# Kernel optimization log

Hardware: AMD Instinct MI355X
Metric: run time of the kernel (lower is better)

Reference implementation:

```python
import jax, jax.numpy as jnp
import numpy as np
from jax import lax

EPSILON = 1e-12


def _sobel_kernels(n1=1, n2=2, n3=2):
    Sx = np.asarray([[[-n1, 0, n1], [-n2, 0, n2], [-n1, 0, n1]],
                     [[-n2, 0, n2], [-n3 * n2, 0, n3 * n2], [-n2, 0, n2]],
                     [[-n1, 0, n1], [-n2, 0, n2], [-n1, 0, n1]]])
    Sy = np.asarray([[[-n1, -n2, -n1], [0, 0, 0], [n1, n2, n1]],
                     [[-n2, -n3 * n2, -n2], [0, 0, 0], [n2, n3 * n2, n2]],
                     [[-n1, -n2, -n1], [0, 0, 0], [n1, n2, n1]]])
    Sz = np.asarray([[[-n1, -n2, -n1], [-n2, -n3 * n2, -n2], [-n1, -n2, -n1]],
                     [[0, 0, 0], [0, 0, 0], [0, 0, 0]],
                     [[n1, n2, n1], [n2, n3 * n2, n2], [n1, n2, n1]]])
    Sd11 = np.asarray([[[0, n1, n2], [-n1, 0, n1], [-n2, -n1, 0]],
                       [[0, n2, n2 * n3], [-n2, 0, n2], [-n2 * n3, -n2, 0]],
                       [[0, n1, n2], [-n1, 0, n1], [-n2, -n1, 0]]])
    Sd12 = np.asarray([[[-n2, -n1, 0], [-n1, 0, n1], [0, n1, n2]],
                       [[-n2 * n3, -n2, 0], [-n2, 0, n2], [0, n2, n2 * n3]],
                       [[-n2, -n1, 0], [-n1, 0, n1], [0, n1, n2]]])
    Sd21 = Sd11.T
    Sd22 = Sd12.T
    Sd31 = np.asarray([-S.T for S in Sd11.T])
    Sd32 = np.asarray([S.T for S in Sd12.T])
    ks = np.stack([Sx, Sy, Sz, Sd11, Sd12, Sd21, Sd22, Sd31, Sd32]).astype(np.float32)
    return jnp.asarray(ks[:, None])  # [9, 1, 3, 3, 3] (OIDHW)


_KERNELS = _sobel_kernels(1, 2, 2)


def _edge_magnitude(img):
    # img: [B, C, H, W, D]. Per-channel convs are summed over C in the original;
    # by linearity of conv, sum channels first, then run all 9 stencils at once.
    C = img.shape[1]
    x = jnp.sum(img, axis=1, keepdims=True)  # [B, 1, H, W, D]
    g = lax.conv_general_dilated(
        x, _KERNELS, window_strides=(1, 1, 1), padding='SAME',
        dimension_numbers=('NCDHW', 'OIDHW', 'NCDHW'))  # [B, 9, H, W, D]
    mag = jnp.sqrt(jnp.sum(g * g, axis=1, keepdims=True) + EPSILON)
    return mag / C  # (1/C) * sqrt(sum_sq + eps), matches operator precedence


def setup_inputs() -> dict:
    key = jax.random.key(0)
    k1, k2 = jax.random.split(key)
    shape = (2, 2, 128, 128, 128)
    y = jax.random.normal(k1, shape, dtype=jnp.float32)
    yp = jax.random.normal(k2, shape, dtype=jnp.float32)
    return {"y": y, "yp": yp}


def reference(y, yp):
    y_edge = _edge_magnitude(y)
    yp_edge = _edge_magnitude(yp)
    return jnp.mean((y_edge - yp_edge) ** 2)  # nn.MSELoss default 'mean'
```

## Files before the change

kernel.cpp:

```cpp
#include <hip/hip_runtime.h>


namespace {

typedef float v2f __attribute__((ext_vector_type(2)));

constexpr int ZDIM = 128, YDIM = 128, XDIM = 128;
constexpr int TX = 64, TY = 4, ZC = 16;
constexpr int OTW = 62;
constexpr int NXT = 3;
constexpr int YX = YDIM * XDIM;
constexpr size_t CS = (size_t)ZDIM * YX;
constexpr float INV_N = 1.0f / 4194304.0f;

__device__ __forceinline__ float bperm(int addr, float v) {
  return __int_as_float(__builtin_amdgcn_ds_bpermute(addr, __float_as_int(v)));
}

__device__ __forceinline__ v2f vfma(v2f a, v2f b, v2f c) {
  return __builtin_elementwise_fma(a, b, c);
}

__device__ __forceinline__ v2f vsplat(float x) { v2f r = {x, x}; return r; }

__device__ __forceinline__ v2f emag_ss(const v2f* __restrict__ Ca,
                                       const v2f* __restrict__ Cb,
                                       const v2f* __restrict__ Cc) {
  const v2f two = vsplat(2.0f);
  const v2f g1  = vfma(two, Cb[0], Ca[0] + Cc[0]);
  const v2f g2  = vfma(two, Cb[1], Ca[1] + Cc[1]);
  const v2f g3  = Cc[2] - Ca[2];
  const v2f Azx = vfma(two, Cb[3], Ca[3] + Cc[3]);
  const v2f Azy = vfma(two, Cb[4], Ca[4] + Cc[4]);
  const v2f Axz = Cc[5] - Ca[5];
  const v2f Axy = g2 - Cb[1];
  const v2f Ayx = g1 - Cb[0];
  const v2f Ayz = Cc[6] - Ca[6];
  const v2f g4 = Azx - Azy, g5 = Azx + Azy;
  const v2f g6 = Axz - Axy, g7 = Axz + Axy;
  const v2f g8 = Ayx - Ayz, g9 = Ayx + Ayz;
  v2f s = vfma(g1, g1, vsplat(1e-12f));
  s = vfma(g2, g2, s); s = vfma(g3, g3, s);
  s = vfma(g4, g4, s); s = vfma(g5, g5, s);
  s = vfma(g6, g6, s); s = vfma(g7, g7, s);
  s = vfma(g8, g8, s); s = vfma(g9, g9, s);
  return s;
}

__global__ __launch_bounds__(256)
void gme_loss_kernel(const float* __restrict__ y,
                     const float* __restrict__ yp,
                     float* __restrict__ out) {
  const int lane = threadIdx.x;
  const int ty   = threadIdx.y;
  const int tid  = ty * TX + lane;

  const int bx = blockIdx.x;
  const int t  = bx % NXT;
  const int yt = bx / NXT;
  const int yy = yt * TY + ty;
  const int z0 = blockIdx.y * ZC;
  const int b  = blockIdx.z;

  const float* Y0 = y  + (size_t)b * 2 * CS;
  const float* Y1 = Y0 + CS;
  const float* P0 = yp + (size_t)b * 2 * CS;
  const float* P1 = P0 + CS;

  const int  X0  = OTW * t - 1;
  const int  xg  = X0 + lane;
  const int  xgc = xg < 0 ? 0 : (xg > XDIM - 1 ? XDIM - 1 : xg);
  const bool xok = (unsigned)xg < (unsigned)XDIM;
  const bool eok = xok && (lane >= 1) && (lane <= OTW);
  const float xmask = xok ? 1.0f : 0.0f;
  const float emask = eok ? 1.0f : 0.0f;

  const int yM = yy > 0 ? yy - 1 : 0;
  const int yP = yy < YDIM - 1 ? yy + 1 : YDIM - 1;
  const int voxM = yM * XDIM + xgc;
  const int voxC = yy * XDIM + xgc;
  const int voxP = yP * XDIM + xgc;
  const float mm = (yy > 0) ? 1.0f : 0.0f;
  const float mp = (yy < YDIM - 1) ? 1.0f : 0.0f;

  const int addrL = (lane > 0 ? lane - 1 : 0) << 2;
  const int addrR = (lane < TX - 1 ? lane + 1 : TX - 1) << 2;

  v2f pf[3][6];
  v2f K[3][7] = {};
  float acc = 0.0f;

  auto loadRaw = [&](int buf, int zc) {
    const int zca = zc < 0 ? 0 : (zc > ZDIM - 1 ? ZDIM - 1 : zc);
    const int o   = zca * YX;
    v2f a0, a1, b0, b1, c0, c1;
    a0.x = Y0[o + voxM]; a0.y = P0[o + voxM];
    a1.x = Y1[o + voxM]; a1.y = P1[o + voxM];
    b0.x = Y0[o + voxC]; b0.y = P0[o + voxC];
    b1.x = Y1[o + voxC]; b1.y = P1[o + voxC];
    c0.x = Y0[o + voxP]; c0.y = P0[o + voxP];
    c1.x = Y1[o + voxP]; c1.y = P1[o + voxP];
    pf[buf][0] = a0; pf[buf][1] = a1;
    pf[buf][2] = b0; pf[buf][3] = b1;
    pf[buf][4] = c0; pf[buf][5] = c1;
  };

  loadRaw(0, z0 - 1);
  loadRaw(1, z0);

#pragma unroll 6
  for (int j = 0; j < ZC + 2; ++j) {
    loadRaw((j + 2) % 3, z0 + 1 + j);

    const int   zc = z0 - 1 + j;
    const float fz = ((unsigned)zc < (unsigned)ZDIM) ? 1.0f : 0.0f;
    const v2f* q = pf[j % 3];
    const v2f sm = (q[0] + q[1]) * vsplat(fz * mm);
    const v2f sc = (q[2] + q[3]) * vsplat(fz);
    const v2f sp = (q[4] + q[5]) * vsplat(fz * mp);

    const v2f tt = sm + sp;
    v2f ys = vfma(vsplat(2.0f), sc, tt);
    v2f yd = sp - sm;
    v2f ye = tt + sc;
    ys *= xmask; yd *= xmask; ye *= xmask;

    v2f ysL, ysR, ydL, ydR, yeL, yeR;
    ysL.x = bperm(addrL, ys.x); ysL.y = bperm(addrL, ys.y);
    ysR.x = bperm(addrR, ys.x); ysR.y = bperm(addrR, ys.y);
    ydL.x = bperm(addrL, yd.x); ydL.y = bperm(addrL, yd.y);
    ydR.x = bperm(addrR, yd.x); ydR.y = bperm(addrR, yd.y);
    yeL.x = bperm(addrL, ye.x); yeL.y = bperm(addrL, ye.y);
    yeR.x = bperm(addrR, ye.x); yeR.y = bperm(addrR, ye.y);

    v2f* C = K[j % 3];
    const v2f tS = ysL + ysR, tD = ydL + ydR, tE = yeL + yeR;
    C[0] = ysR - ysL;
    C[2] = vfma(vsplat(2.0f), ys, tS);
    C[6] = tS + ys;
    C[1] = vfma(vsplat(2.0f), yd, tD);
    C[4] = tD + yd;
    C[3] = yeR - yeL;
    C[5] = vfma(vsplat(2.0f), ye, tE);

    if (j >= 2) {
      const v2f ss = emag_ss(K[(j + 1) % 3], K[(j + 2) % 3], C);
      const float my = __builtin_amdgcn_sqrtf(ss.x);
      const float mp2 = __builtin_amdgcn_sqrtf(ss.y);
      float d = 0.5f * (my - mp2);
      d *= emask;
      acc = __builtin_fmaf(d, d, acc);
    }
  }

  __shared__ float red[4];
#pragma unroll
  for (int off = 32; off > 0; off >>= 1) acc += __shfl_down(acc, off);
  if (lane == 0) red[ty] = acc;
  __syncthreads();
  if (tid == 0) {
    const float s = (red[0] + red[1] + red[2] + red[3]) * INV_N;
    atomicAdd(out, s);
  }
}

}

extern "C" void kernel_launch(void* const* d_in, const int* in_sizes, int n_in,
                              void* d_out, int out_size, void* d_ws, size_t ws_size,
                              hipStream_t stream) {
  const float* y  = (const float*)d_in[0];
  const float* yp = (const float*)d_in[1];
  float* out = (float*)d_out;

  hipMemsetAsync(out, 0, sizeof(float), stream);

  dim3 block(TX, TY, 1);
  dim3 grid(NXT * (YDIM / TY),
            ZDIM / ZC,
            2);
  gme_loss_kernel<<<grid, block, 0, stream>>>(y, yp, out);
}
```

Before: 114.8 us.

## Process two x-voxels per lane with float2 loads, eliminating x-tile halo overlap

Each lane now owns two adjacent x voxels and loads them as float2, so a 64-lane row covers the full 128-wide x extent and the three overlapping x tiles with halos go away. The y and yp fields are processed as separate packed pairs, and neighbor exchange needs only one bpermute per direction instead of two. This removes redundant halo loads and compute, but doubles the per-thread register footprint and cuts the grid by a factor of three, which may hurt occupancy and latency hiding.

```diff
diff --git a/kernel.cpp b/kernel.cpp
--- a/kernel.cpp
+++ b/kernel.cpp
@@ -7,10 +7,9 @@
 
 constexpr int ZDIM = 128, YDIM = 128, XDIM = 128;
 constexpr int TX = 64, TY = 4, ZC = 16;
-constexpr int OTW = 62;
-constexpr int NXT = 3;
-constexpr int YX = YDIM * XDIM;
-constexpr size_t CS = (size_t)ZDIM * YX;
+constexpr int XW  = XDIM / 2;
+constexpr int YX2 = YDIM * XW;
+constexpr size_t CS2 = (size_t)ZDIM * YX2;
 constexpr float INV_N = 1.0f / 4194304.0f;
 
 __device__ __forceinline__ float bperm(int addr, float v) {
@@ -55,54 +54,58 @@
   const int ty   = threadIdx.y;
   const int tid  = ty * TX + lane;
 
-  const int bx = blockIdx.x;
-  const int t  = bx % NXT;
-  const int yt = bx / NXT;
-  const int yy = yt * TY + ty;
+  const int yy = blockIdx.x * TY + ty;
   const int z0 = blockIdx.y * ZC;
   const int b  = blockIdx.z;
 
-  const float* Y0 = y  + (size_t)b * 2 * CS;
-  const float* Y1 = Y0 + CS;
-  const float* P0 = yp + (size_t)b * 2 * CS;
-  const float* P1 = P0 + CS;
-
-  const int  X0  = OTW * t - 1;
-  const int  xg  = X0 + lane;
-  const int  xgc = xg < 0 ? 0 : (xg > XDIM - 1 ? XDIM - 1 : xg);
-  const bool xok = (unsigned)xg < (unsigned)XDIM;
-  const bool eok = xok && (lane >= 1) && (lane <= OTW);
-  const float xmask = xok ? 1.0f : 0.0f;
-  const float emask = eok ? 1.0f : 0.0f;
+  const v2f* Y0 = (const v2f*)y  + (size_t)b * 2 * CS2;
+  const v2f* Y1 = Y0 + CS2;
+  const v2f* P0 = (const v2f*)yp + (size_t)b * 2 * CS2;
+  const v2f* P1 = P0 + CS2;
 
   const int yM = yy > 0 ? yy - 1 : 0;
   const int yP = yy < YDIM - 1 ? yy + 1 : YDIM - 1;
-  const int voxM = yM * XDIM + xgc;
-  const int voxC = yy * XDIM + xgc;
-  const int voxP = yP * XDIM + xgc;
+  const int oM = yM * XW + lane;
+  const int oC = yy * XW + lane;
+  const int oP = yP * XW + lane;
   const float mm = (yy > 0) ? 1.0f : 0.0f;
   const float mp = (yy < YDIM - 1) ? 1.0f : 0.0f;
 
   const int addrL = (lane > 0 ? lane - 1 : 0) << 2;
   const int addrR = (lane < TX - 1 ? lane + 1 : TX - 1) << 2;
+  const float lz = (lane == 0) ? 0.0f : 1.0f;
+  const float rz = (lane == TX - 1) ? 0.0f : 1.0f;
 
-  v2f pf[3][6];
-  v2f K[3][7] = {};
-  float acc = 0.0f;
+  v2f pf[3][12];
+  v2f KY[2][7], KP[2][7];
+  v2f accv = {0.0f, 0.0f};
 
   auto loadRaw = [&](int buf, int zc) {
     const int zca = zc < 0 ? 0 : (zc > ZDIM - 1 ? ZDIM - 1 : zc);
-    const int o   = zca * YX;
-    v2f a0, a1, b0, b1, c0, c1;
-    a0.x = Y0[o + voxM]; a0.y = P0[o + voxM];
-    a1.x = Y1[o + voxM]; a1.y = P1[o + voxM];
-    b0.x = Y0[o + voxC]; b0.y = P0[o + voxC];
-    b1.x = Y1[o + voxC]; b1.y = P1[o + voxC];
-    c0.x = Y0[o + voxP]; c0.y = P0[o + voxP];
-    c1.x = Y1[o + voxP]; c1.y = P1[o + voxP];
-    pf[buf][0] = a0; pf[buf][1] = a1;
-    pf[buf][2] = b0; pf[buf][3] = b1;
-    pf[buf][4] = c0; pf[buf][5] = c1;
+    const int o   = zca * YX2;
+    pf[buf][0]  = Y0[o + oM]; pf[buf][1]  = Y1[o + oM];
+    pf[buf][2]  = P0[o + oM]; pf[buf][3]  = P1[o + oM];
+    pf[buf][4]  = Y0[o + oC]; pf[buf][5]  = Y1[o + oC];
+    pf[buf][6]  = P0[o + oC]; pf[buf][7]  = P1[o + oC];
+    pf[buf][8]  = Y0[o + oP]; pf[buf][9]  = Y1[o + oP];
+    pf[buf][10] = P0[o + oP]; pf[buf][11] = P1[o + oP];
+  };
+
+  auto combos = [&](v2f ys, v2f yd, v2f ye, v2f* __restrict__ C) {
+    const float ysl = bperm(addrL, ys.y) * lz, ysr = bperm(addrR, ys.x) * rz;
+    const float ydl = bperm(addrL, yd.y) * lz, ydr = bperm(addrR, yd.x) * rz;
+    const float yel = bperm(addrL, ye.y) * lz, yer = bperm(addrR, ye.x) * rz;
+    const v2f ysL = {ysl, ys.x}, ysR = {ys.y, ysr};
+    const v2f ydL = {ydl, yd.x}, ydR = {yd.y, ydr};
+    const v2f yeL = {yel, ye.x}, yeR = {ye.y, yer};
+    const v2f tS = ysL + ysR, tD = ydL + ydR, tE = yeL + yeR;
+    C[0] = ysR - ysL;
+    C[2] = vfma(vsplat(2.0f), ys, tS);
+    C[6] = tS + ys;
+    C[1] = vfma(vsplat(2.0f), yd, tD);
+    C[4] = tD + yd;
+    C[3] = yeR - yeL;
+    C[5] = vfma(vsplat(2.0f), ye, tE);
   };
 
   loadRaw(0, z0 - 1);
@@ -115,45 +118,38 @@
     const int   zc = z0 - 1 + j;
     const float fz = ((unsigned)zc < (unsigned)ZDIM) ? 1.0f : 0.0f;
     const v2f* q = pf[j % 3];
-    const v2f sm = (q[0] + q[1]) * vsplat(fz * mm);
-    const v2f sc = (q[2] + q[3]) * vsplat(fz);
-    const v2f sp = (q[4] + q[5]) * vsplat(fz * mp);
+    const v2f smY = (q[0] + q[1])  * vsplat(fz * mm);
+    const v2f smP = (q[2] + q[3])  * vsplat(fz * mm);
+    const v2f scY = (q[4] + q[5])  * vsplat(fz);
+    const v2f scP = (q[6] + q[7])  * vsplat(fz);
+    const v2f spY = (q[8] + q[9])  * vsplat(fz * mp);
+    const v2f spP = (q[10] + q[11]) * vsplat(fz * mp);
 
-    const v2f tt = sm + sp;
-    v2f ys = vfma(vsplat(2.0f), sc, tt);
-    v2f yd = sp - sm;
-    v2f ye = tt + sc;
-    ys *= xmask; yd *= xmask; ye *= xmask;
-
-    v2f ysL, ysR, ydL, ydR, yeL, yeR;
-    ysL.x = bperm(addrL, ys.x); ysL.y = bperm(addrL, ys.y);
-    ysR.x = bperm(addrR, ys.x); ysR.y = bperm(addrR, ys.y);
-    ydL.x = bperm(addrL, yd.x); ydL.y = bperm(addrL, yd.y);
-    ydR.x = bperm(addrR, yd.x); ydR.y = bperm(addrR, yd.y);
-    yeL.x = bperm(addrL, ye.x); yeL.y = bperm(addrL, ye.y);
-    yeR.x = bperm(addrR, ye.x); yeR.y = bperm(addrR, ye.y);
-
-    v2f* C = K[j % 3];
-    const v2f tS = ysL + ysR, tD = ydL + ydR, tE = yeL + yeR;
-    C[0] = ysR - ysL;
-    C[2] = vfma(vsplat(2.0f), ys, tS);
-    C[6] = tS + ys;
-    C[1] = vfma(vsplat(2.0f), yd, tD);
-    C[4] = tD + yd;
-    C[3] = yeR - yeL;
-    C[5] = vfma(vsplat(2.0f), ye, tE);
+    v2f Cy[7], Cp[7];
+    {
+      const v2f tt = smY + spY;
+      combos(vfma(vsplat(2.0f), scY, tt), spY - smY, tt + scY, Cy);
+    }
+    {
+      const v2f tt = smP + spP;
+      combos(vfma(vsplat(2.0f), scP, tt), spP - smP, tt + scP, Cp);
+    }
 
     if (j >= 2) {
-      const v2f ss = emag_ss(K[(j + 1) % 3], K[(j + 2) % 3], C);
-      const float my = __builtin_amdgcn_sqrtf(ss.x);
-      const float mp2 = __builtin_amdgcn_sqrtf(ss.y);
-      float d = 0.5f * (my - mp2);
-      d *= emask;
-      acc = __builtin_fmaf(d, d, acc);
+      const v2f ssY = emag_ss(KY[j % 2], KY[(j + 1) % 2], Cy);
+      const v2f ssP = emag_ss(KP[j % 2], KP[(j + 1) % 2], Cp);
+      v2f d;
+      d.x = 0.5f * (__builtin_amdgcn_sqrtf(ssY.x) - __builtin_amdgcn_sqrtf(ssP.x));
+      d.y = 0.5f * (__builtin_amdgcn_sqrtf(ssY.y) - __builtin_amdgcn_sqrtf(ssP.y));
+      accv = vfma(d, d, accv);
     }
+
+#pragma unroll
+    for (int k = 0; k < 7; ++k) { KY[j % 2][k] = Cy[k]; KP[j % 2][k] = Cp[k]; }
   }
 
   __shared__ float red[4];
+  float acc = accv.x + accv.y;
 #pragma unroll
   for (int off = 32; off > 0; off >>= 1) acc += __shfl_down(acc, off);
   if (lane == 0) red[ty] = acc;
@@ -176,7 +172,7 @@
   hipMemsetAsync(out, 0, sizeof(float), stream);
 
   dim3 block(TX, TY, 1);
-  dim3 grid(NXT * (YDIM / TY),
+  dim3 grid(YDIM / TY,
             ZDIM / ZC,
             2);
   gme_loss_kernel<<<grid, block, 0, stream>>>(y, yp, out);
```

New measurement: 107.2 us. -6.6%, faster.
